# Optimization experiments

Measured on AMD Instinct MI355X. Metric: run time of the kernel, lower is better.

Reference implementation:

```python
import jax, jax.numpy as jnp
import numpy as np


def setup_inputs() -> dict:
    key = jax.random.key(0)
    k1, k2, k3, k4 = jax.random.split(key, 4)
    B, To, Tw, D = 64, 36, 32, 512  # Bo == Bw == B required by .diag()
    o = jax.random.normal(k1, (B, To, D), dtype=jnp.float32)
    u = jax.random.normal(k2, (B, To, D), dtype=jnp.float32)
    w = jax.random.normal(k3, (B, Tw, D), dtype=jnp.float32)
    mask = jax.random.randint(k4, (B, Tw), 0, 2).astype(jnp.int32)  # 1 = masked
    return {"o": o, "u": u, "w": w, "mask": mask}


def reference(o, u, w, mask):
    # o: (Bo, To, D) contextualized object feats; u: (Bo, To, D) uncontextualized;
    # w: (Bw, Tw, D) caption word feats; mask: (Bw, Tw) with 1 = padded word.
    D = w.shape[-1]
    # Original computes sum(Kw * Ku, 4) over a broadcast (Bw,Bo,Tw,To,D) tensor;
    # that is exactly a cross-batch contraction -> einsum.
    scores = jnp.einsum('wtd,bod->wbto', w, u) / jnp.sqrt(jnp.asarray(D, jnp.float32))
    att = jax.nn.softmax(scores, axis=3)              # softmax over objects To
    att_V_o = jnp.einsum('wbto,bod->wbtd', att, o)    # attention-weighted objects
    logits = jnp.einsum('wbtd,wtd->wbt', att_V_o, w)  # (Bw, Bo, Tw)
    log_sm = jax.nn.log_softmax(logits, axis=1)       # InfoNCE over Bo
    keep = 1.0 - mask.astype(log_sm.dtype)            # (Bw, Tw), 1 = valid word
    log_sm = log_sm * keep[:, None, :]
    num_non_mask = jnp.sum(keep, axis=1)[:, None, None]  # (Bw, 1, 1)
    log_sm = log_sm / (num_non_mask + 1e-6)
    loss_mat = jnp.sum(log_sm, axis=2)                # (Bw, Bo)
    loss = -jnp.mean(jnp.diagonal(loss_mat))
    return (loss, att, att_V_o)
```

## Files before the change

kernel.cpp:

```cpp
#include <hip/hip_runtime.h>

#define BB 64
#define TO 36
#define TW 32
#define DD 512

typedef short short8 __attribute__((ext_vector_type(8)));
typedef float floatx4 __attribute__((ext_vector_type(4)));


__device__ __forceinline__ unsigned short f2bf(float f) {
  unsigned int x = __builtin_bit_cast(unsigned int, f);
  x += 0x7FFFu + ((x >> 16) & 1u);
  return (unsigned short)(x >> 16);
}

__device__ __forceinline__ short8 ld8(const unsigned short* p) {
  return __builtin_bit_cast(short8, *(const uint4*)p);
}

__global__ __launch_bounds__(256) void prep_kernel(
    const float* __restrict__ o_g, const float* __restrict__ u_g,
    const float* __restrict__ w_g, unsigned short* __restrict__ wbf,
    unsigned short* __restrict__ ubf, unsigned short* __restrict__ ot) {
  const int blk = blockIdx.x, tid = threadIdx.x;
  if (blk < 512) {
    int i8 = blk * 256 + tid;
    const float4* src = (const float4*)w_g;
    float4 f0 = src[i8 * 2], f1 = src[i8 * 2 + 1];
    uint4 d;
    d.x = (unsigned)f2bf(f0.x) | ((unsigned)f2bf(f0.y) << 16);
    d.y = (unsigned)f2bf(f0.z) | ((unsigned)f2bf(f0.w) << 16);
    d.z = (unsigned)f2bf(f1.x) | ((unsigned)f2bf(f1.y) << 16);
    d.w = (unsigned)f2bf(f1.z) | ((unsigned)f2bf(f1.w) << 16);
    ((uint4*)wbf)[i8] = d;
  } else if (blk < 1088) {
    int i8 = (blk - 512) * 256 + tid;
    const float4* src = (const float4*)u_g;
    float4 f0 = src[i8 * 2], f1 = src[i8 * 2 + 1];
    uint4 d;
    d.x = (unsigned)f2bf(f0.x) | ((unsigned)f2bf(f0.y) << 16);
    d.y = (unsigned)f2bf(f0.z) | ((unsigned)f2bf(f0.w) << 16);
    d.z = (unsigned)f2bf(f1.x) | ((unsigned)f2bf(f1.y) << 16);
    d.w = (unsigned)f2bf(f1.z) | ((unsigned)f2bf(f1.w) << 16);
    ((uint4*)ubf)[i8] = d;
  } else {
    int t2 = (blk - 1088) * 256 + tid;
    int b = t2 >> 9, d = t2 & 511;
    uint4 bufv[8];
    unsigned short* buf = (unsigned short*)bufv;
#pragma unroll
    for (int o = 0; o < 64; ++o)
      buf[o] = (o < TO) ? f2bf(o_g[((b * TO + o) << 9) + d]) : (unsigned short)0;
    uint4* dst = (uint4*)(ot + ((size_t)((b << 9) + d) << 6));
#pragma unroll
    for (int i = 0; i < 8; ++i) dst[i] = bufv[i];
  }
}

__global__ __launch_bounds__(64) void main_kernel(
    const float* __restrict__ w_g,
    const unsigned short* __restrict__ wbf,
    const unsigned short* __restrict__ ubf,
    const unsigned short* __restrict__ ot,
    float* __restrict__ logits_ws,
    float* __restrict__ att_out,
    float* __restrict__ attV_out) {
  const int b = blockIdx.x, wb = blockIdx.y;
  const int lane = threadIdx.x;
  const int c = lane & 15;
  const int q = lane >> 4;

  __shared__ unsigned short att_s[TW][72];
  {
    unsigned int* p = (unsigned int*)&att_s[0][0];
#pragma unroll
    for (int i = 0; i < 18; ++i) p[lane + 64 * i] = 0u;
  }

  const unsigned short* wbp = wbf + (size_t)wb * TW * DD;
  const unsigned short* ubp = ubf + (size_t)b * TO * DD;

  floatx4 acc[2][3];
#pragma unroll
  for (int i = 0; i < 2; ++i)
#pragma unroll
    for (int j = 0; j < 3; ++j) acc[i][j] = (floatx4){0.f, 0.f, 0.f, 0.f};

  int r2 = 32 + c; if (r2 > 35) r2 = 35;
#pragma unroll 2
  for (int kk = 0; kk < 16; ++kk) {
    int k0 = kk * 32 + q * 8;
    short8 a0 = ld8(wbp + c * DD + k0);
    short8 a1 = ld8(wbp + (16 + c) * DD + k0);
    short8 u0 = ld8(ubp + c * DD + k0);
    short8 u1 = ld8(ubp + (16 + c) * DD + k0);
    short8 u2 = ld8(ubp + r2 * DD + k0);
    acc[0][0] = __builtin_amdgcn_mfma_f32_16x16x32_bf16(a0, u0, acc[0][0], 0, 0, 0);
    acc[0][1] = __builtin_amdgcn_mfma_f32_16x16x32_bf16(a0, u1, acc[0][1], 0, 0, 0);
    acc[0][2] = __builtin_amdgcn_mfma_f32_16x16x32_bf16(a0, u2, acc[0][2], 0, 0, 0);
    acc[1][0] = __builtin_amdgcn_mfma_f32_16x16x32_bf16(a1, u0, acc[1][0], 0, 0, 0);
    acc[1][1] = __builtin_amdgcn_mfma_f32_16x16x32_bf16(a1, u1, acc[1][1], 0, 0, 0);
    acc[1][2] = __builtin_amdgcn_mfma_f32_16x16x32_bf16(a1, u2, acc[1][2], 0, 0, 0);
  }

  const float scale = 0.04419417382415922f;
  float attv[2][3][4];
  const bool v2 = (c < 4);
#pragma unroll
  for (int mt = 0; mt < 2; ++mt) {
#pragma unroll
    for (int reg = 0; reg < 4; ++reg) {
      float s0 = acc[mt][0][reg] * scale;
      float s1 = acc[mt][1][reg] * scale;
      float s2 = acc[mt][2][reg] * scale;
      float m = fmaxf(s0, s1);
      if (v2) m = fmaxf(m, s2);
#pragma unroll
      for (int off = 1; off < 16; off <<= 1) m = fmaxf(m, __shfl_xor(m, off));
      float e0 = __expf(s0 - m);
      float e1 = __expf(s1 - m);
      float e2 = v2 ? __expf(s2 - m) : 0.f;
      float sum = e0 + e1 + e2;
#pragma unroll
      for (int off = 1; off < 16; off <<= 1) sum += __shfl_xor(sum, off);
      float inv = 1.f / sum;
      attv[mt][0][reg] = e0 * inv;
      attv[mt][1][reg] = e1 * inv;
      attv[mt][2][reg] = e2 * inv;
    }
  }

  float* attb = att_out + (size_t)(wb * BB + b) * TW * TO;
#pragma unroll
  for (int mt = 0; mt < 2; ++mt)
#pragma unroll
    for (int reg = 0; reg < 4; ++reg) {
      int t = mt * 16 + q * 4 + reg;
#pragma unroll
      for (int nt = 0; nt < 3; ++nt) {
        int oo = nt * 16 + c;
        if (oo < TO) {
          attb[t * TO + oo] = attv[mt][nt][reg];
          att_s[t][oo] = f2bf(attv[mt][nt][reg]);
        }
      }
    }
  __syncthreads();

  short8 a2[2][2];
#pragma unroll
  for (int mt = 0; mt < 2; ++mt)
#pragma unroll
    for (int kk = 0; kk < 2; ++kk)
      a2[mt][kk] = ld8(&att_s[mt * 16 + c][kk * 32 + q * 8]);

  const unsigned short* otp = ot + (size_t)b * DD * 64;
  const float* wrow = w_g + (size_t)wb * TW * DD;
  float* avb = attV_out + (size_t)(wb * BB + b) * TW * DD;
  float lp[2][4] = {{0.f, 0.f, 0.f, 0.f}, {0.f, 0.f, 0.f, 0.f}};

#pragma unroll 2
  for (int nt2 = 0; nt2 < 32; ++nt2) {
    int d0 = nt2 * 16;
    short8 b0 = ld8(otp + (d0 + c) * 64 + q * 8);
    short8 b1 = ld8(otp + (d0 + c) * 64 + 32 + q * 8);
#pragma unroll
    for (int mt = 0; mt < 2; ++mt) {
      floatx4 a = (floatx4){0.f, 0.f, 0.f, 0.f};
      a = __builtin_amdgcn_mfma_f32_16x16x32_bf16(a2[mt][0], b0, a, 0, 0, 0);
      a = __builtin_amdgcn_mfma_f32_16x16x32_bf16(a2[mt][1], b1, a, 0, 0, 0);
#pragma unroll
      for (int reg = 0; reg < 4; ++reg) {
        int t = mt * 16 + q * 4 + reg;
        float v = a[reg];
        avb[t * DD + d0 + c] = v;
        lp[mt][reg] = fmaf(v, wrow[t * DD + d0 + c], lp[mt][reg]);
      }
    }
  }

#pragma unroll
  for (int mt = 0; mt < 2; ++mt)
#pragma unroll
    for (int reg = 0; reg < 4; ++reg) {
      float s = lp[mt][reg];
#pragma unroll
      for (int off = 1; off < 16; off <<= 1) s += __shfl_xor(s, off);
      if (c == 0) {
        int t = mt * 16 + q * 4 + reg;
        logits_ws[(size_t)(wb * BB + b) * TW + t] = s;
      }
    }
}

__global__ __launch_bounds__(64) void loss_kernel(
    const float* __restrict__ logits, const int* __restrict__ mask,
    float* __restrict__ out) {
  int wb = blockIdx.x, lane = threadIdx.x;
  const float* lrow = logits + ((size_t)wb * BB + lane) * TW;
  float accv = 0.f, nnm = 0.f;
  for (int t = 0; t < TW; ++t) {
    float v = lrow[t];
    float m = v;
#pragma unroll
    for (int off = 1; off < 64; off <<= 1) m = fmaxf(m, __shfl_xor(m, off));
    float e = __expf(v - m);
    float s = e;
#pragma unroll
    for (int off = 1; off < 64; off <<= 1) s += __shfl_xor(s, off);
    float diag = __shfl(v, wb);
    float lsm = diag - m - __logf(s);
    float keep = 1.f - (float)mask[wb * TW + t];
    accv += lsm * keep;
    nnm += keep;
  }
  if (lane == 0) atomicAdd(out, -(accv / (nnm + 1e-6f)) * (1.f / 64.f));
}

extern "C" void kernel_launch(void* const* d_in, const int* in_sizes, int n_in,
                              void* d_out, int out_size, void* d_ws, size_t ws_size,
                              hipStream_t stream) {
  const float* o_g = (const float*)d_in[0];
  const float* u_g = (const float*)d_in[1];
  const float* w_g = (const float*)d_in[2];
  const int* mask  = (const int*)d_in[3];

  float* out = (float*)d_out;
  float* att_out  = out + 1;
  float* attV_out = out + 1 + (size_t)BB * BB * TW * TO;

  char* ws = (char*)d_ws;
  unsigned short* wbf = (unsigned short*)(ws + 0);
  unsigned short* ubf = (unsigned short*)(ws + 2097152);
  unsigned short* ot  = (unsigned short*)(ws + 4456448);
  float* logits       = (float*)(ws + 8650752);

  hipMemsetAsync(d_out, 0, sizeof(float), stream);
  prep_kernel<<<1216, 256, 0, stream>>>(o_g, u_g, w_g, wbf, ubf, ot);
  main_kernel<<<dim3(BB, BB), 64, 0, stream>>>(w_g, wbf, ubf, ot, logits,
                                               att_out, attV_out);
  loss_kernel<<<BB, 64, 0, stream>>>(logits, mask, out);
}
```

Baseline: 466.6 us.

## Split main kernel across two waves per block and use nontemporal output stores

Each block now runs two wavefronts, and each wave handles 16 of the 32 caption words. The per-wave shared attention tile is split to match, so each wave keeps its own register accumulators and softmax work. Outputs for att and att_V_o are written with nontemporal stores so the large streaming writes do not pollute the cache, and the second-stage loop unroll grows from 2 to 4. The goal is more parallelism and latency hiding on a kernel bound by output writes. The cost is that the u and o_t loads are now duplicated across the two waves.

Result: slower. 532.9 us (+14.2%).

```diff
diff --git a/kernel.cpp b/kernel.cpp
--- a/kernel.cpp
+++ b/kernel.cpp
@@ -58,7 +58,7 @@
   }
 }
 
-__global__ __launch_bounds__(64) void main_kernel(
+__global__ __launch_bounds__(128) void main_kernel(
     const float* __restrict__ w_g,
     const unsigned short* __restrict__ wbf,
     const unsigned short* __restrict__ ubf,
@@ -67,131 +67,105 @@
     float* __restrict__ att_out,
     float* __restrict__ attV_out) {
   const int b = blockIdx.x, wb = blockIdx.y;
-  const int lane = threadIdx.x;
+  const int tid = threadIdx.x;
+  const int wave = tid >> 6;
+  const int lane = tid & 63;
   const int c = lane & 15;
   const int q = lane >> 4;
 
-  __shared__ unsigned short att_s[TW][72];
+  __shared__ unsigned short att_s[2][16][72];
   {
-    unsigned int* p = (unsigned int*)&att_s[0][0];
-#pragma unroll
-    for (int i = 0; i < 18; ++i) p[lane + 64 * i] = 0u;
-  }
-
-  const unsigned short* wbp = wbf + (size_t)wb * TW * DD;
+    unsigned int* p = (unsigned int*)&att_s[wave][0][0];
+#pragma unroll
+    for (int i = 0; i < 9; ++i) p[lane + 64 * i] = 0u;
+  }
+
+  const unsigned short* wbp = wbf + (size_t)wb * TW * DD + (size_t)wave * 16 * DD;
   const unsigned short* ubp = ubf + (size_t)b * TO * DD;
 
-  floatx4 acc[2][3];
-#pragma unroll
-  for (int i = 0; i < 2; ++i)
-#pragma unroll
-    for (int j = 0; j < 3; ++j) acc[i][j] = (floatx4){0.f, 0.f, 0.f, 0.f};
+  floatx4 acc[3];
+#pragma unroll
+  for (int j = 0; j < 3; ++j) acc[j] = (floatx4){0.f, 0.f, 0.f, 0.f};
 
   int r2 = 32 + c; if (r2 > 35) r2 = 35;
 #pragma unroll 2
   for (int kk = 0; kk < 16; ++kk) {
     int k0 = kk * 32 + q * 8;
     short8 a0 = ld8(wbp + c * DD + k0);
-    short8 a1 = ld8(wbp + (16 + c) * DD + k0);
     short8 u0 = ld8(ubp + c * DD + k0);
     short8 u1 = ld8(ubp + (16 + c) * DD + k0);
     short8 u2 = ld8(ubp + r2 * DD + k0);
-    acc[0][0] = __builtin_amdgcn_mfma_f32_16x16x32_bf16(a0, u0, acc[0][0], 0, 0, 0);
-    acc[0][1] = __builtin_amdgcn_mfma_f32_16x16x32_bf16(a0, u1, acc[0][1], 0, 0, 0);
-    acc[0][2] = __builtin_amdgcn_mfma_f32_16x16x32_bf16(a0, u2, acc[0][2], 0, 0, 0);
-    acc[1][0] = __builtin_amdgcn_mfma_f32_16x16x32_bf16(a1, u0, acc[1][0], 0, 0, 0);
-    acc[1][1] = __builtin_amdgcn_mfma_f32_16x16x32_bf16(a1, u1, acc[1][1], 0, 0, 0);
-    acc[1][2] = __builtin_amdgcn_mfma_f32_16x16x32_bf16(a1, u2, acc[1][2], 0, 0, 0);
+    acc[0] = __builtin_amdgcn_mfma_f32_16x16x32_bf16(a0, u0, acc[0], 0, 0, 0);
+    acc[1] = __builtin_amdgcn_mfma_f32_16x16x32_bf16(a0, u1, acc[1], 0, 0, 0);
+    acc[2] = __builtin_amdgcn_mfma_f32_16x16x32_bf16(a0, u2, acc[2], 0, 0, 0);
   }
 
   const float scale = 0.04419417382415922f;
-  float attv[2][3][4];
   const bool v2 = (c < 4);
-#pragma unroll
-  for (int mt = 0; mt < 2; ++mt) {
-#pragma unroll
-    for (int reg = 0; reg < 4; ++reg) {
-      float s0 = acc[mt][0][reg] * scale;
-      float s1 = acc[mt][1][reg] * scale;
-      float s2 = acc[mt][2][reg] * scale;
-      float m = fmaxf(s0, s1);
-      if (v2) m = fmaxf(m, s2);
-#pragma unroll
-      for (int off = 1; off < 16; off <<= 1) m = fmaxf(m, __shfl_xor(m, off));
-      float e0 = __expf(s0 - m);
-      float e1 = __expf(s1 - m);
-      float e2 = v2 ? __expf(s2 - m) : 0.f;
-      float sum = e0 + e1 + e2;
-#pragma unroll
-      for (int off = 1; off < 16; off <<= 1) sum += __shfl_xor(sum, off);
-      float inv = 1.f / sum;
-      attv[mt][0][reg] = e0 * inv;
-      attv[mt][1][reg] = e1 * inv;
-      attv[mt][2][reg] = e2 * inv;
-    }
-  }
-
   float* attb = att_out + (size_t)(wb * BB + b) * TW * TO;
 #pragma unroll
-  for (int mt = 0; mt < 2; ++mt)
-#pragma unroll
-    for (int reg = 0; reg < 4; ++reg) {
-      int t = mt * 16 + q * 4 + reg;
-#pragma unroll
-      for (int nt = 0; nt < 3; ++nt) {
-        int oo = nt * 16 + c;
-        if (oo < TO) {
-          attb[t * TO + oo] = attv[mt][nt][reg];
-          att_s[t][oo] = f2bf(attv[mt][nt][reg]);
-        }
-      }
-    }
+  for (int reg = 0; reg < 4; ++reg) {
+    float s0 = acc[0][reg] * scale;
+    float s1 = acc[1][reg] * scale;
+    float s2 = acc[2][reg] * scale;
+    float m = fmaxf(s0, s1);
+    if (v2) m = fmaxf(m, s2);
+#pragma unroll
+    for (int off = 1; off < 16; off <<= 1) m = fmaxf(m, __shfl_xor(m, off));
+    float e0 = __expf(s0 - m);
+    float e1 = __expf(s1 - m);
+    float e2 = v2 ? __expf(s2 - m) : 0.f;
+    float sum = e0 + e1 + e2;
+#pragma unroll
+    for (int off = 1; off < 16; off <<= 1) sum += __shfl_xor(sum, off);
+    float inv = 1.f / sum;
+    float a0v = e0 * inv, a1v = e1 * inv, a2v = e2 * inv;
+    int t = wave * 16 + q * 4 + reg;
+    __builtin_nontemporal_store(a0v, &attb[t * TO + c]);
+    __builtin_nontemporal_store(a1v, &attb[t * TO + 16 + c]);
+    if (v2) __builtin_nontemporal_store(a2v, &attb[t * TO + 32 + c]);
+    att_s[wave][q * 4 + reg][c] = f2bf(a0v);
+    att_s[wave][q * 4 + reg][16 + c] = f2bf(a1v);
+    if (v2) att_s[wave][q * 4 + reg][32 + c] = f2bf(a2v);
+  }
   __syncthreads();
 
-  short8 a2[2][2];
-#pragma unroll
-  for (int mt = 0; mt < 2; ++mt)
-#pragma unroll
-    for (int kk = 0; kk < 2; ++kk)
-      a2[mt][kk] = ld8(&att_s[mt * 16 + c][kk * 32 + q * 8]);
+  short8 a2f[2];
+  a2f[0] = ld8(&att_s[wave][c][q * 8]);
+  a2f[1] = ld8(&att_s[wave][c][32 + q * 8]);
 
   const unsigned short* otp = ot + (size_t)b * DD * 64;
-  const float* wrow = w_g + (size_t)wb * TW * DD;
-  float* avb = attV_out + (size_t)(wb * BB + b) * TW * DD;
-  float lp[2][4] = {{0.f, 0.f, 0.f, 0.f}, {0.f, 0.f, 0.f, 0.f}};
-
-#pragma unroll 2
+  const float* wrow = w_g + (size_t)wb * TW * DD + (size_t)wave * 16 * DD;
+  float* avb = attV_out + (size_t)(wb * BB + b) * TW * DD + (size_t)wave * 16 * DD;
+  float lp[4] = {0.f, 0.f, 0.f, 0.f};
+
+#pragma unroll 4
   for (int nt2 = 0; nt2 < 32; ++nt2) {
     int d0 = nt2 * 16;
     short8 b0 = ld8(otp + (d0 + c) * 64 + q * 8);
     short8 b1 = ld8(otp + (d0 + c) * 64 + 32 + q * 8);
-#pragma unroll
-    for (int mt = 0; mt < 2; ++mt) {
-      floatx4 a = (floatx4){0.f, 0.f, 0.f, 0.f};
-      a = __builtin_amdgcn_mfma_f32_16x16x32_bf16(a2[mt][0], b0, a, 0, 0, 0);
-      a = __builtin_amdgcn_mfma_f32_16x16x32_bf16(a2[mt][1], b1, a, 0, 0, 0);
-#pragma unroll
-      for (int reg = 0; reg < 4; ++reg) {
-        int t = mt * 16 + q * 4 + reg;
-        float v = a[reg];
-        avb[t * DD + d0 + c] = v;
-        lp[mt][reg] = fmaf(v, wrow[t * DD + d0 + c], lp[mt][reg]);
-      }
+    floatx4 a = (floatx4){0.f, 0.f, 0.f, 0.f};
+    a = __builtin_amdgcn_mfma_f32_16x16x32_bf16(a2f[0], b0, a, 0, 0, 0);
+    a = __builtin_amdgcn_mfma_f32_16x16x32_bf16(a2f[1], b1, a, 0, 0, 0);
+#pragma unroll
+    for (int reg = 0; reg < 4; ++reg) {
+      int t = q * 4 + reg;
+      float v = a[reg];
+      __builtin_nontemporal_store(v, &avb[t * DD + d0 + c]);
+      lp[reg] = fmaf(v, wrow[t * DD + d0 + c], lp[reg]);
     }
   }
 
 #pragma unroll
-  for (int mt = 0; mt < 2; ++mt)
-#pragma unroll
-    for (int reg = 0; reg < 4; ++reg) {
-      float s = lp[mt][reg];
-#pragma unroll
-      for (int off = 1; off < 16; off <<= 1) s += __shfl_xor(s, off);
-      if (c == 0) {
-        int t = mt * 16 + q * 4 + reg;
-        logits_ws[(size_t)(wb * BB + b) * TW + t] = s;
-      }
+  for (int reg = 0; reg < 4; ++reg) {
+    float s = lp[reg];
+#pragma unroll
+    for (int off = 1; off < 16; off <<= 1) s += __shfl_xor(s, off);
+    if (c == 0) {
+      int t = wave * 16 + q * 4 + reg;
+      logits_ws[(size_t)(wb * BB + b) * TW + t] = s;
     }
+  }
 }
 
 __global__ __launch_bounds__(64) void loss_kernel(
@@ -238,7 +212,7 @@
 
   hipMemsetAsync(d_out, 0, sizeof(float), stream);
   prep_kernel<<<1216, 256, 0, stream>>>(o_g, u_g, w_g, wbf, ubf, ot);
-  main_kernel<<<dim3(BB, BB), 64, 0, stream>>>(w_g, wbf, ubf, ot, logits,
-                                               att_out, attV_out);
+  main_kernel<<<dim3(BB, BB), 128, 0, stream>>>(w_g, wbf, ubf, ot, logits,
+                                                att_out, attV_out);
   loss_kernel<<<BB, 64, 0, stream>>>(logits, mask, out);
 }
```
